# Performance work log

Hardware: AMD Instinct MI355X
Metric: run time of the kernel (lower is better)

The kernel has to match this reference:

```python
import jax, jax.numpy as jnp
import numpy as np

B, D, H, O, E = 1048576, 17, 8, 6, 4  # batch, input_dim, expert_hidden, output_dim, n_clusters
G1, G2 = 64, 32  # gating hidden dims


def setup_inputs() -> dict:
    key = jax.random.key(0)
    ks = jax.random.split(key, 14)
    def w(k, shape, fan_in):
        return (jax.random.normal(k, shape, jnp.float32) / jnp.sqrt(jnp.float32(fan_in)))
    return {
        "x": jax.random.normal(ks[0], (B, D), jnp.float32),
        # per-expert MLP params, stacked on leading expert axis E
        "eW1": w(ks[1], (E, D, H), D), "eb1": w(ks[2], (E, H), D),
        "eW2": w(ks[3], (E, H, H), H), "eb2": w(ks[4], (E, H), H),
        "eW3": w(ks[5], (E, H, O), H), "eb3": w(ks[6], (E, O), H),
        # gating classifier params
        "gW1": w(ks[7], (D, G1), D), "gb1": w(ks[8], (G1,), D),
        "gW2": w(ks[9], (G1, G2), G1), "gb2": w(ks[10], (G2,), G1),
        "gW3": w(ks[11], (G2, E), G2), "gb3": w(ks[12], (E,), G2),
    }


def reference(x, eW1, eb1, eW2, eb2, eW3, eb3, gW1, gb1, gW2, gb2, gW3, gb3):
    # gating network: 17 -> 64 -> 32 -> 4 logits
    h = jax.nn.relu(x @ gW1 + gb1)
    h = jax.nn.relu(h @ gW2 + gb2)
    gating_logits = h @ gW3 + gb3  # [B, E]
    selected = jnp.argmax(gating_logits, axis=1)  # [B] hard routing
    # all experts computed (as in the original), stacked over expert axis
    e = jax.nn.relu(jnp.einsum('bi,eih->beh', x, eW1) + eb1)   # [B, E, H]
    e = jax.nn.relu(jnp.einsum('beh,ehk->bek', e, eW2) + eb2)  # [B, E, H]
    eo = jnp.einsum('bek,eko->beo', e, eW3) + eb3              # [B, E, O]
    # gather the selected expert's output per sample
    predictions = jnp.take_along_axis(eo, selected[:, None, None], axis=1)[:, 0, :]  # [B, O]
    return predictions, gating_logits
```

## Files before the change

kernel.cpp:

```cpp
#include <hip/hip_runtime.h>

#define BTOT 1048576
#define D 17
#define H 8
#define OUT 6
#define E 4
#define G1 64
#define G2 32

__global__ __launch_bounds__(256) void hybrid_ruc_kernel(
    const float* __restrict__ x,
    const float* __restrict__ eW1, const float* __restrict__ eb1,
    const float* __restrict__ eW2, const float* __restrict__ eb2,
    const float* __restrict__ eW3, const float* __restrict__ eb3,
    const float* __restrict__ gW1, const float* __restrict__ gb1,
    const float* __restrict__ gW2, const float* __restrict__ gb2,
    const float* __restrict__ gW3, const float* __restrict__ gb3,
    float* __restrict__ out)
{
    __shared__ float sx[256 * D];
    const int tid = threadIdx.x;
    const long long bbase = (long long)blockIdx.x * 256;

    #pragma unroll
    for (int k = 0; k < D; ++k) {
        int t = tid + k * 256;
        sx[t] = x[bbase * D + t];
    }
    __syncthreads();

    float xr[D];
    #pragma unroll
    for (int i = 0; i < D; ++i) xr[i] = sx[tid * D + i];

    float h2[G2];
    #pragma unroll
    for (int j = 0; j < G2; ++j) h2[j] = gb2[j];

    #pragma unroll 1
    for (int jt = 0; jt < G1 / 16; ++jt) {
        float h1t[16];
        #pragma unroll
        for (int c = 0; c < 16; ++c) h1t[c] = gb1[jt * 16 + c];
        #pragma unroll
        for (int i = 0; i < D; ++i) {
            const float xi = xr[i];
            const float* w1row = gW1 + i * G1 + jt * 16;
            #pragma unroll
            for (int c = 0; c < 16; ++c)
                h1t[c] = __builtin_fmaf(xi, w1row[c], h1t[c]);
        }
        #pragma unroll
        for (int c = 0; c < 16; ++c) {
            const float hv = fmaxf(h1t[c], 0.0f);
            const float* w2row = gW2 + (jt * 16 + c) * G2;
            #pragma unroll
            for (int j = 0; j < G2; ++j)
                h2[j] = __builtin_fmaf(hv, w2row[j], h2[j]);
        }
    }

    float lg[E];
    #pragma unroll
    for (int e = 0; e < E; ++e) lg[e] = gb3[e];
    #pragma unroll
    for (int j = 0; j < G2; ++j) {
        const float hv = fmaxf(h2[j], 0.0f);
        #pragma unroll
        for (int e = 0; e < E; ++e)
            lg[e] = __builtin_fmaf(hv, gW3[j * E + e], lg[e]);
    }

    int sel = 0;
    float best = lg[0];
    #pragma unroll
    for (int e = 1; e < E; ++e) {
        if (lg[e] > best) { best = lg[e]; sel = e; }
    }

    float pred[OUT];
    #pragma unroll
    for (int o = 0; o < OUT; ++o) pred[o] = 0.0f;

    #pragma unroll 1
    for (int e = 0; e < E; ++e) {
        float t1[H];
        #pragma unroll
        for (int h = 0; h < H; ++h) t1[h] = eb1[e * H + h];
        #pragma unroll
        for (int i = 0; i < D; ++i) {
            const float xi = xr[i];
            const float* w = eW1 + e * D * H + i * H;
            #pragma unroll
            for (int h = 0; h < H; ++h)
                t1[h] = __builtin_fmaf(xi, w[h], t1[h]);
        }
        float t2[H];
        #pragma unroll
        for (int h = 0; h < H; ++h) t2[h] = eb2[e * H + h];
        #pragma unroll
        for (int k = 0; k < H; ++k) {
            const float tv = fmaxf(t1[k], 0.0f);
            const float* w = eW2 + e * H * H + k * H;
            #pragma unroll
            for (int h = 0; h < H; ++h)
                t2[h] = __builtin_fmaf(tv, w[h], t2[h]);
        }
        float po[OUT];
        #pragma unroll
        for (int o = 0; o < OUT; ++o) po[o] = eb3[e * OUT + o];
        #pragma unroll
        for (int k = 0; k < H; ++k) {
            const float tv = fmaxf(t2[k], 0.0f);
            const float* w = eW3 + e * H * OUT + k * OUT;
            #pragma unroll
            for (int o = 0; o < OUT; ++o)
                po[o] = __builtin_fmaf(tv, w[o], po[o]);
        }
        #pragma unroll
        for (int o = 0; o < OUT; ++o)
            pred[o] = (sel == e) ? po[o] : pred[o];
    }

    const long long b = bbase + tid;
    #pragma unroll
    for (int o = 0; o < OUT; ++o) out[b * OUT + o] = pred[o];
    float* lout = out + (long long)BTOT * OUT;
    #pragma unroll
    for (int e = 0; e < E; ++e) lout[b * E + e] = lg[e];
}

extern "C" void kernel_launch(void* const* d_in, const int* in_sizes, int n_in,
                              void* d_out, int out_size, void* d_ws, size_t ws_size,
                              hipStream_t stream) {
    const float* x   = (const float*)d_in[0];
    const float* eW1 = (const float*)d_in[1];
    const float* eb1 = (const float*)d_in[2];
    const float* eW2 = (const float*)d_in[3];
    const float* eb2 = (const float*)d_in[4];
    const float* eW3 = (const float*)d_in[5];
    const float* eb3 = (const float*)d_in[6];
    const float* gW1 = (const float*)d_in[7];
    const float* gb1 = (const float*)d_in[8];
    const float* gW2 = (const float*)d_in[9];
    const float* gb2 = (const float*)d_in[10];
    const float* gW3 = (const float*)d_in[11];
    const float* gb3 = (const float*)d_in[12];
    float* out = (float*)d_out;

    dim3 grid(BTOT / 256), block(256);
    hipLaunchKernelGGL(hybrid_ruc_kernel, grid, block, 0, stream,
                       x, eW1, eb1, eW2, eb2, eW3, eb3,
                       gW1, gb1, gW2, gb2, gW3, gb3, out);
}
```

Baseline: 218.1 us.

## Compute only the selected expert using per-block LDS-staged expert weights

Instead of evaluating all four expert MLPs and selecting the output, each thread evaluates only the expert chosen by its argmax. Expert weights and biases are staged in shared memory in a padded per-expert layout (stride 296), so threads with different selections can index them and use vector reads. This cuts expert FLOPs by about 4x and replaces uniform scalar weight loads with divergent LDS reads, at the cost of extra shared-memory setup per block and possible bank conflicts. Results are unchanged because the skipped experts never reach the output.

```diff
diff --git a/kernel.cpp b/kernel.cpp
--- a/kernel.cpp
+++ b/kernel.cpp
@@ -7,6 +7,8 @@
 #define E 4
 #define G1 64
 #define G2 32
+
+#define WSTR 296
 
 __global__ __launch_bounds__(256) void hybrid_ruc_kernel(
     const float* __restrict__ x,
@@ -19,6 +21,8 @@
     float* __restrict__ out)
 {
     __shared__ float sx[256 * D];
+    __shared__ __align__(16) float swl[E * WSTR];
+
     const int tid = threadIdx.x;
     const long long bbase = (long long)blockIdx.x * 256;
 
@@ -26,6 +30,29 @@
     for (int k = 0; k < D; ++k) {
         int t = tid + k * 256;
         sx[t] = x[bbase * D + t];
+    }
+
+    for (int t = tid; t < E * D * H; t += 256) {
+        swl[(t / 136) * WSTR + (t % 136)] = eW1[t];
+    }
+    {
+        int t = tid;
+        if (t < E * H * H) {
+            swl[(t / 64) * WSTR + 144 + (t % 64)] = eW2[t];
+        }
+    }
+    if (tid < E * H * OUT) {
+        int e = tid / 48, r = tid % 48, k = r / 6, o = r % 6;
+        swl[e * WSTR + 216 + k * 8 + o] = eW3[tid];
+    }
+    if (tid < E * H) {
+        swl[(tid / 8) * WSTR + 136 + (tid % 8)] = eb1[tid];
+    }
+    if (tid < E * H) {
+        swl[(tid / 8) * WSTR + 208 + (tid % 8)] = eb2[tid];
+    }
+    if (tid < E * OUT) {
+        swl[(tid / 6) * WSTR + 280 + (tid % 6)] = eb3[tid];
     }
     __syncthreads();
 
@@ -78,48 +105,69 @@
         if (lg[e] > best) { best = lg[e]; sel = e; }
     }
 
+    const float* wl = &swl[sel * WSTR];
+
+    float t1[H];
+    {
+        float4 ba = *(const float4*)(wl + 136);
+        float4 bb = *(const float4*)(wl + 140);
+        t1[0] = ba.x; t1[1] = ba.y; t1[2] = ba.z; t1[3] = ba.w;
+        t1[4] = bb.x; t1[5] = bb.y; t1[6] = bb.z; t1[7] = bb.w;
+    }
+    #pragma unroll
+    for (int i = 0; i < D; ++i) {
+        const float xi = xr[i];
+        float4 wa = *(const float4*)(wl + i * 8);
+        float4 wb = *(const float4*)(wl + i * 8 + 4);
+        t1[0] = __builtin_fmaf(xi, wa.x, t1[0]);
+        t1[1] = __builtin_fmaf(xi, wa.y, t1[1]);
+        t1[2] = __builtin_fmaf(xi, wa.z, t1[2]);
+        t1[3] = __builtin_fmaf(xi, wa.w, t1[3]);
+        t1[4] = __builtin_fmaf(xi, wb.x, t1[4]);
+        t1[5] = __builtin_fmaf(xi, wb.y, t1[5]);
+        t1[6] = __builtin_fmaf(xi, wb.z, t1[6]);
+        t1[7] = __builtin_fmaf(xi, wb.w, t1[7]);
+    }
+
+    float t2[H];
+    {
+        float4 ba = *(const float4*)(wl + 208);
+        float4 bb = *(const float4*)(wl + 212);
+        t2[0] = ba.x; t2[1] = ba.y; t2[2] = ba.z; t2[3] = ba.w;
+        t2[4] = bb.x; t2[5] = bb.y; t2[6] = bb.z; t2[7] = bb.w;
+    }
+    #pragma unroll
+    for (int k = 0; k < H; ++k) {
+        const float tv = fmaxf(t1[k], 0.0f);
+        float4 wa = *(const float4*)(wl + 144 + k * 8);
+        float4 wb = *(const float4*)(wl + 144 + k * 8 + 4);
+        t2[0] = __builtin_fmaf(tv, wa.x, t2[0]);
+        t2[1] = __builtin_fmaf(tv, wa.y, t2[1]);
+        t2[2] = __builtin_fmaf(tv, wa.z, t2[2]);
+        t2[3] = __builtin_fmaf(tv, wa.w, t2[3]);
+        t2[4] = __builtin_fmaf(tv, wb.x, t2[4]);
+        t2[5] = __builtin_fmaf(tv, wb.y, t2[5]);
+        t2[6] = __builtin_fmaf(tv, wb.z, t2[6]);
+        t2[7] = __builtin_fmaf(tv, wb.w, t2[7]);
+    }
+
     float pred[OUT];
-    #pragma unroll
-    for (int o = 0; o < OUT; ++o) pred[o] = 0.0f;
-
-    #pragma unroll 1
-    for (int e = 0; e < E; ++e) {
-        float t1[H];
-        #pragma unroll
-        for (int h = 0; h < H; ++h) t1[h] = eb1[e * H + h];
-        #pragma unroll
-        for (int i = 0; i < D; ++i) {
-            const float xi = xr[i];
-            const float* w = eW1 + e * D * H + i * H;
-            #pragma unroll
-            for (int h = 0; h < H; ++h)
-                t1[h] = __builtin_fmaf(xi, w[h], t1[h]);
-        }
-        float t2[H];
-        #pragma unroll
-        for (int h = 0; h < H; ++h) t2[h] = eb2[e * H + h];
-        #pragma unroll
-        for (int k = 0; k < H; ++k) {
-            const float tv = fmaxf(t1[k], 0.0f);
-            const float* w = eW2 + e * H * H + k * H;
-            #pragma unroll
-            for (int h = 0; h < H; ++h)
-                t2[h] = __builtin_fmaf(tv, w[h], t2[h]);
-        }
-        float po[OUT];
-        #pragma unroll
-        for (int o = 0; o < OUT; ++o) po[o] = eb3[e * OUT + o];
-        #pragma unroll
-        for (int k = 0; k < H; ++k) {
-            const float tv = fmaxf(t2[k], 0.0f);
-            const float* w = eW3 + e * H * OUT + k * OUT;
-            #pragma unroll
-            for (int o = 0; o < OUT; ++o)
-                po[o] = __builtin_fmaf(tv, w[o], po[o]);
-        }
-        #pragma unroll
-        for (int o = 0; o < OUT; ++o)
-            pred[o] = (sel == e) ? po[o] : pred[o];
+    {
+        float4 ba = *(const float4*)(wl + 280);
+        pred[0] = ba.x; pred[1] = ba.y; pred[2] = ba.z; pred[3] = ba.w;
+        pred[4] = wl[284]; pred[5] = wl[285];
+    }
+    #pragma unroll
+    for (int k = 0; k < H; ++k) {
+        const float tv = fmaxf(t2[k], 0.0f);
+        float4 wa = *(const float4*)(wl + 216 + k * 8);
+        float4 wb = *(const float4*)(wl + 216 + k * 8 + 4);
+        pred[0] = __builtin_fmaf(tv, wa.x, pred[0]);
+        pred[1] = __builtin_fmaf(tv, wa.y, pred[1]);
+        pred[2] = __builtin_fmaf(tv, wa.z, pred[2]);
+        pred[3] = __builtin_fmaf(tv, wa.w, pred[3]);
+        pred[4] = __builtin_fmaf(tv, wb.x, pred[4]);
+        pred[5] = __builtin_fmaf(tv, wb.y, pred[5]);
     }
 
     const long long b = bbase + tid;
```

Measured after the change: 196.4 us. -10.0%, faster.
